# Kernel tuning notes

Measured on AMD Instinct MI355X. Metric: run time of the kernel, lower is better.

## Reference

```python
import jax, jax.numpy as jnp
import numpy as np

H = 768          # hidden_size
NH = 12          # num heads
HD = H // NH     # head dim
NEG = -1e9       # stand-in for -inf masked_fill (numerically safe)


def setup_inputs() -> dict:
    key = jax.random.key(0)
    ks = jax.random.split(key, 8)
    B, T = 4, 2048
    s = 0.02
    return {
        "hidden_states": jax.random.normal(ks[0], (B, T, H), jnp.float32),
        "attention_mask": jnp.zeros((B, 1, 1, T), jnp.float32),
        "Wq": jax.random.normal(ks[1], (H, H), jnp.float32) * s,
        "bq": jnp.zeros((H,), jnp.float32),
        "Wk": jax.random.normal(ks[2], (H, H), jnp.float32) * s,
        "bk": jnp.zeros((H,), jnp.float32),
        "Wv": jax.random.normal(ks[3], (H, H), jnp.float32) * s,
        "bv": jnp.zeros((H,), jnp.float32),
    }


def _split_heads(x):
    b, t, _ = x.shape
    return x.reshape(b, t, NH, HD).transpose(0, 2, 1, 3)  # b h t d


def reference(hidden_states, attention_mask, Wq, bq, Wk, bk, Wv, bv):
    q = _split_heads(hidden_states @ Wq.T + bq)
    k = _split_heads(hidden_states @ Wk.T + bk)
    v = _split_heads(hidden_states @ Wv.T + bv)
    T = q.shape[2]
    scores = jnp.einsum('bhid,bhjd->bhij', q, k) / jnp.sqrt(jnp.float32(HD))
    causal = jnp.tril(jnp.ones((T, T), bool))
    scores = jnp.where(causal, scores, NEG) + attention_mask
    probs = jax.nn.softmax(scores, axis=-1)
    out = jnp.einsum('bhij,bhjd->bhid', probs, v)
    b = out.shape[0]
    return out.transpose(0, 2, 1, 3).reshape(b, T, H)  # b t (h d)
```

## Files before the change

### kernel.cpp

```cpp
#include <hip/hip_runtime.h>
#include <hip/hip_bf16.h>

#define Tsz 2048
#define Hsz 768
#define NHsz 12
#define HDsz 64

typedef unsigned short u16;
typedef unsigned int u32;
typedef __attribute__((ext_vector_type(8))) short bf16x8;
typedef __attribute__((ext_vector_type(4))) float f32x4;
typedef __attribute__((ext_vector_type(4))) u16 u16x4;

__device__ __forceinline__ u16 f2bf(float f) {
    union { __hip_bfloat16 h; u16 u; } c;
    c.h = __float2bfloat16(f);
    return c.u;
}

__device__ __forceinline__ void glds16(const void* src, void* ldsbase) {
    __builtin_amdgcn_global_load_lds(
        (const __attribute__((address_space(1))) u32*)src,
        (__attribute__((address_space(3))) u32*)ldsbase, 16, 0, 0);
}

#define BAR() do { asm volatile("" ::: "memory"); \
                   __builtin_amdgcn_s_barrier();  \
                   asm volatile("" ::: "memory"); } while (0)

#define LDSFRAG(base, row, c) \
    (*(const bf16x8*)((const char*)(base) + (row)*128 + ((((c) << 4)) ^ (((row) & 7) << 4))))

__global__ __launch_bounds__(256) void to_bf16(
    const float* __restrict__ X,
    const float* __restrict__ Wq, const float* __restrict__ Wk,
    const float* __restrict__ Wv,
    u16* __restrict__ xb, u16* __restrict__ wb)
{
    const int bx = blockIdx.x, tid = threadIdx.x;
    const float* src;
    u16* dst;
    size_t off;
    if (bx < 768) {
        src = X; dst = xb;
        off = ((size_t)bx * 256 + tid) * 32;
    } else {
        int r = bx - 768;
        int wsel = r / 72, lr = r % 72;
        src = (wsel == 0) ? Wq : (wsel == 1) ? Wk : Wv;
        dst = wb + (size_t)wsel * (Hsz * Hsz);
        off = ((size_t)lr * 256 + tid) * 32;
    }
    #pragma unroll
    for (int c = 0; c < 4; ++c) {
        float4 a = *(const float4*)(src + off + c * 8);
        float4 b = *(const float4*)(src + off + c * 8 + 4);
        bf16x8 v;
        v[0] = (short)f2bf(a.x); v[1] = (short)f2bf(a.y);
        v[2] = (short)f2bf(a.z); v[3] = (short)f2bf(a.w);
        v[4] = (short)f2bf(b.x); v[5] = (short)f2bf(b.y);
        v[6] = (short)f2bf(b.z); v[7] = (short)f2bf(b.w);
        *(bf16x8*)(dst + off + c * 8) = v;
    }
}

__global__ __launch_bounds__(256) void qkv_gemm(
    const u16* __restrict__ xb, const u16* __restrict__ wb,
    const float* __restrict__ bq, const float* __restrict__ bk,
    const float* __restrict__ bv,
    u16* __restrict__ q_ws, u16* __restrict__ k_ws, u16* __restrict__ vt_ws)
{
    const int tid = threadIdx.x;
    const int w = tid >> 6, l = tid & 63, lg = l >> 4, lh = l & 15;
    const int nb = blockIdx.x;
    const int m0 = blockIdx.y * 128;
    const int z = nb / 6;
    const int n0l = (nb % 6) * 128;
    const u16* Wb = wb + (size_t)z * (Hsz * Hsz);
    const float* bias = (z == 0) ? bq : (z == 1) ? bk : bv;

    __shared__ __align__(16) u16 Xs[2][128 * 64];
    __shared__ __align__(16) u16 Ws[2][128 * 64];

    const int wm = w >> 1, wn = w & 1;

    f32x4 acc[4][4];
    #pragma unroll
    for (int i = 0; i < 4; ++i)
        #pragma unroll
        for (int j = 0; j < 4; ++j)
            acc[i][j] = (f32x4){0.f, 0.f, 0.f, 0.f};

    auto stage = [&](int buf, int k0) {
        #pragma unroll
        for (int p = 0; p < 4; ++p) {
            int id = w * 256 + p * 64 + l;
            int r = id >> 3, c8 = id & 7;
            int cswz = c8 ^ (r & 7);
            glds16(xb + (size_t)(m0 + r) * Hsz + k0 + cswz * 8,
                   &Xs[buf][(w * 256 + p * 64) * 8]);
            glds16(Wb + (size_t)(n0l + r) * Hsz + k0 + cswz * 8,
                   &Ws[buf][(w * 256 + p * 64) * 8]);
        }
    };

    stage(0, 0);
    asm volatile("s_waitcnt vmcnt(0)" ::: "memory");
    BAR();

    #pragma unroll 1
    for (int ks = 0; ks < 12; ++ks) {
        const int cur = ks & 1;
        if (ks < 11) {
            stage(cur ^ 1, (ks + 1) * 64);
            asm volatile("s_waitcnt vmcnt(8)" ::: "memory");
        } else {
            asm volatile("s_waitcnt vmcnt(0)" ::: "memory");
        }
        BAR();

        __builtin_amdgcn_s_setprio(1);
        #pragma unroll
        for (int s = 0; s < 2; ++s) {
            bf16x8 af[4], bfr[4];
            #pragma unroll
            for (int tq = 0; tq < 4; ++tq) {
                af[tq]  = LDSFRAG(Xs[cur], wm * 64 + tq * 16 + lh, 4 * s + lg);
                bfr[tq] = LDSFRAG(Ws[cur], wn * 64 + tq * 16 + lh, 4 * s + lg);
            }
            #pragma unroll
            for (int mt = 0; mt < 4; ++mt)
                #pragma unroll
                for (int nt = 0; nt < 4; ++nt)
                    acc[mt][nt] = __builtin_amdgcn_mfma_f32_16x16x32_bf16(
                        af[mt], bfr[nt], acc[mt][nt], 0, 0, 0);
        }
        __builtin_amdgcn_s_setprio(0);
        BAR();
    }

    #pragma unroll
    for (int nt = 0; nt < 4; ++nt) {
        int nloc = n0l + wn * 64 + nt * 16 + lh;
        float bval = bias[nloc];
        int hh = nloc >> 6, d = nloc & 63;
        #pragma unroll
        for (int mt = 0; mt < 4; ++mt) {
            #pragma unroll
            for (int r = 0; r < 4; ++r) {
                int m = m0 + wm * 64 + mt * 16 + lg * 4 + r;
                int bb = m >> 11, t = m & 2047;
                u16 val = f2bf(acc[mt][nt][r] + bval);
                size_t bh = (size_t)(bb * NHsz + hh);
                if (z == 0)      q_ws[(bh * Tsz + t) * HDsz + d] = val;
                else if (z == 1) k_ws[(bh * Tsz + t) * HDsz + d] = val;
                else             vt_ws[(bh * HDsz + d) * Tsz + t] = val;
            }
        }
    }
}

__global__ __launch_bounds__(256) void attn_mfma(
    const u16* __restrict__ q_ws, const u16* __restrict__ k_ws,
    const u16* __restrict__ vt_ws, const float* __restrict__ am,
    float* __restrict__ out)
{
    const int tid = threadIdx.x;
    const int w = tid >> 6, l = tid & 63, lg = l >> 4, lh = l & 15;
    const int bx = blockIdx.x;
    const int h = blockIdx.y, b = blockIdx.z;
    const int bh = b * NHsz + h;

    const u16* Qb = q_ws + (size_t)bh * Tsz * HDsz;
    const u16* Kb = k_ws + (size_t)bh * Tsz * HDsz;
    const u16* Vb = vt_ws + (size_t)bh * HDsz * Tsz;
    const float* amb = am + (size_t)b * Tsz;

    __shared__ __align__(16) u16 Ks[2][64 * 64];
    __shared__ __align__(16) u16 Vs[2][64 * 64];
    __shared__ __align__(16) u16 Ps[4][16 * 64];
    __shared__ __align__(16) float ambs[Tsz];

    const float LOG2E  = 1.44269504f;
    const float SCALE2 = 0.125f * 1.44269504f;
    const f32x4 zero4 = {0.f, 0.f, 0.f, 0.f};
    u16* myP = &Ps[w][0];
    const int srcbase = l & 0x30;
    const int qo = lg * 4;

    #pragma unroll
    for (int i = 0; i < 2; ++i)
        glds16(amb + (size_t)(i * 256 + tid) * 4, ambs + (i * 256 + w * 64) * 4);
    asm volatile("s_waitcnt vmcnt(0)" ::: "memory");
    __syncthreads();
    #pragma unroll
    for (int i = 0; i < 8; ++i) ambs[tid * 8 + i] *= LOG2E;
    __syncthreads();

    #pragma unroll 1
    for (int ph = 0; ph < 2; ++ph) {
        const int qt = (ph == 0) ? (16 + bx) : (15 - bx);
        const int q0 = qt * 64 + w * 16;
        const int qrow = q0 + lh;

        #pragma unroll
        for (int p = 0; p < 2; ++p) {
            int id = w * 128 + p * 64 + l;
            int r = id >> 3, c8 = id & 7;
            int cswz = c8 ^ (r & 7);
            glds16(Kb + (size_t)r * HDsz + cswz * 8, &Ks[0][(w * 128 + p * 64) * 8]);
            glds16(Vb + (size_t)r * Tsz + cswz * 8, &Vs[0][(w * 128 + p * 64) * 8]);
        }
        bf16x8 qf0 = *(const bf16x8*)(Qb + (size_t)(q0 + lh) * HDsz + lg * 8);
        bf16x8 qf1 = *(const bf16x8*)(Qb + (size_t)(q0 + lh) * HDsz + lg * 8 + 32);
        asm volatile("s_waitcnt vmcnt(0)" ::: "memory");
        BAR();

        f32x4 o[4];
        #pragma unroll
        for (int n = 0; n < 4; ++n) o[n] = zero4;
        float m2 = -1e30f, l2 = 0.f;

        #pragma unroll 1
        for (int kt = 0; kt <= qt; ++kt) {
            const int cur = kt & 1;
            const int kv0 = kt * 64;

            if (kt < qt) {
                const int kv1 = kv0 + 64;
                #pragma unroll
                for (int p = 0; p < 2; ++p) {
                    int id = w * 128 + p * 64 + l;
                    int r = id >> 3, c8 = id & 7;
                    int cswz = c8 ^ (r & 7);
                    glds16(Kb + (size_t)(kv1 + r) * HDsz + cswz * 8,
                           &Ks[cur ^ 1][(w * 128 + p * 64) * 8]);
                    glds16(Vb + (size_t)r * Tsz + kv1 + cswz * 8,
                           &Vs[cur ^ 1][(w * 128 + p * 64) * 8]);
                }
                asm volatile("s_waitcnt vmcnt(4)" ::: "memory");
            } else {
                asm volatile("s_waitcnt vmcnt(0)" ::: "memory");
            }
            BAR();

            const u16* Ksb = &Ks[cur][0];
            const u16* Vsb = &Vs[cur][0];
            const bool diag = (kt == qt);

            f32x4 st[4];
            __builtin_amdgcn_s_setprio(1);
            if (!diag) {
                #pragma unroll
                for (int n = 0; n < 4; ++n) {
                    int row = n * 16 + lh;
                    bf16x8 kf0 = LDSFRAG(Ksb, row, lg);
                    bf16x8 kf1 = LDSFRAG(Ksb, row, 4 + lg);
                    f32x4 c = __builtin_amdgcn_mfma_f32_16x16x32_bf16(kf0, qf0, zero4, 0, 0, 0);
                    st[n] = __builtin_amdgcn_mfma_f32_16x16x32_bf16(kf1, qf1, c, 0, 0, 0);
                }
            } else {
                #pragma unroll
                for (int n = 0; n < 4; ++n) {
                    st[n] = zero4;
                    if (n <= w) {
                        int row = n * 16 + lh;
                        bf16x8 kf0 = LDSFRAG(Ksb, row, lg);
                        bf16x8 kf1 = LDSFRAG(Ksb, row, 4 + lg);
                        f32x4 c = __builtin_amdgcn_mfma_f32_16x16x32_bf16(kf0, qf0, zero4, 0, 0, 0);
                        st[n] = __builtin_amdgcn_mfma_f32_16x16x32_bf16(kf1, qf1, c, 0, 0, 0);
                    }
                }
            }
            __builtin_amdgcn_s_setprio(0);

            float pvv[16];
            float mx = -1e30f;
            if (!diag) {
                #pragma unroll
                for (int n = 0; n < 4; ++n) {
                    f32x4 a4 = *(const f32x4*)(ambs + kv0 + n * 16 + lg * 4);
                    #pragma unroll
                    for (int r = 0; r < 4; ++r) {
                        float sv = fmaf(st[n][r], SCALE2, a4[r]);
                        pvv[n * 4 + r] = sv;
                        mx = fmaxf(mx, sv);
                    }
                }
            } else {
                #pragma unroll
                for (int n = 0; n < 4; ++n) {
                    f32x4 a4 = *(const f32x4*)(ambs + kv0 + n * 16 + lg * 4);
                    #pragma unroll
                    for (int r = 0; r < 4; ++r) {
                        int kvj = kv0 + n * 16 + lg * 4 + r;
                        float sv = (kvj > qrow) ? -1e30f : fmaf(st[n][r], SCALE2, a4[r]);
                        pvv[n * 4 + r] = sv;
                        mx = fmaxf(mx, sv);
                    }
                }
            }
            mx = fmaxf(mx, __shfl_xor(mx, 16));
            mx = fmaxf(mx, __shfl_xor(mx, 32));

            const bool norescale = __all(mx <= m2 + 8.0f);
            float mn = m2;
            if (!norescale) mn = fmaxf(m2, mx);

            float ps = 0.f;
            #pragma unroll
            for (int i = 0; i < 16; ++i) {
                float p = exp2f(pvv[i] - mn);
                pvv[i] = p;
                ps += p;
            }
            ps += __shfl_xor(ps, 16);
            ps += __shfl_xor(ps, 32);

            if (norescale) {
                l2 += ps;
            } else {
                float corr = exp2f(m2 - mn);
                m2 = mn;
                l2 = l2 * corr + ps;
                float co[4];
                #pragma unroll
                for (int r = 0; r < 4; ++r)
                    co[r] = __shfl(corr, srcbase | (qo + r));
                #pragma unroll
                for (int n = 0; n < 4; ++n)
                    #pragma unroll
                    for (int r = 0; r < 4; ++r)
                        o[n][r] *= co[r];
            }

            #pragma unroll
            for (int n = 0; n < 4; ++n) {
                u16x4 v;
                v[0] = f2bf(pvv[n * 4 + 0]); v[1] = f2bf(pvv[n * 4 + 1]);
                v[2] = f2bf(pvv[n * 4 + 2]); v[3] = f2bf(pvv[n * 4 + 3]);
                int chunk = 2 * n + (lg >> 1);
                int byteoff = lh * 128 + ((chunk ^ (lh & 7)) << 4) + ((lg & 1) << 3);
                *(u16x4*)((char*)myP + byteoff) = v;
            }

            const int smaxv = (diag && w < 2) ? 0 : 1;
            __builtin_amdgcn_s_setprio(1);
            #pragma unroll
            for (int s = 0; s < 2; ++s) {
                if (s <= smaxv) {
                    int chunk = (4 * s + lg) ^ (lh & 7);
                    bf16x8 pf = *(const bf16x8*)((const char*)myP + lh * 128 + (chunk << 4));
                    #pragma unroll
                    for (int n = 0; n < 4; ++n) {
                        bf16x8 vf = LDSFRAG(Vsb, n * 16 + lh, 4 * s + lg);
                        o[n] = __builtin_amdgcn_mfma_f32_16x16x32_bf16(pf, vf, o[n], 0, 0, 0);
                    }
                }
            }
            __builtin_amdgcn_s_setprio(0);
            BAR();
        }

        float linv[4];
        #pragma unroll
        for (int r = 0; r < 4; ++r)
            linv[r] = 1.0f / __shfl(l2, srcbase | (qo + r));
        float* ob = out + ((size_t)(b * Tsz + q0 + qo)) * Hsz + h * HDsz + lh;
        #pragma unroll
        for (int r = 0; r < 4; ++r)
            #pragma unroll
            for (int n = 0; n < 4; ++n)
                ob[r * Hsz + n * 16] = o[n][r] * linv[r];
    }
}

extern "C" void kernel_launch(void* const* d_in, const int* in_sizes, int n_in,
                              void* d_out, int out_size, void* d_ws, size_t ws_size,
                              hipStream_t stream) {
    const float* X  = (const float*)d_in[0];
    const float* am = (const float*)d_in[1];
    const float* Wq = (const float*)d_in[2];
    const float* bq = (const float*)d_in[3];
    const float* Wk = (const float*)d_in[4];
    const float* bk = (const float*)d_in[5];
    const float* Wv = (const float*)d_in[6];
    const float* bv = (const float*)d_in[7];
    float* out = (float*)d_out;

    const size_t per = (size_t)8192 * Hsz;
    u16* q_ws  = (u16*)d_ws;
    u16* k_ws  = q_ws + per;
    u16* vt_ws = k_ws + per;

    u16* xb = (u16*)d_out;
    u16* wb = xb + per;

    to_bf16<<<dim3(984), 256, 0, stream>>>(X, Wq, Wk, Wv, xb, wb);

    dim3 g1(18, 64);
    qkv_gemm<<<g1, 256, 0, stream>>>(xb, wb, bq, bk, bv, q_ws, k_ws, vt_ws);

    dim3 g2(16, NHsz, 4);
    attn_mfma<<<g2, 256, 0, stream>>>(q_ws, k_ws, vt_ws, am, out);
}
```

Measured before the change: 150.3 us.

## Redistribute P fragments via cross-lane shuffles and swizzle attention grid mapping

```diff
diff --git a/kernel.cpp b/kernel.cpp
--- a/kernel.cpp
+++ b/kernel.cpp
@@ -167,8 +167,11 @@
 {
     const int tid = threadIdx.x;
     const int w = tid >> 6, l = tid & 63, lg = l >> 4, lh = l & 15;
-    const int bx = blockIdx.x;
-    const int h = blockIdx.y, b = blockIdx.z;
+    const int wg = blockIdx.x;
+    const int swz = (wg & 7) * 96 + (wg >> 3);
+    const int bx = swz & 15;
+    const int grp = swz >> 4;
+    const int h = grp % NHsz, b = grp / NHsz;
     const int bh = b * NHsz + h;
 
     const u16* Qb = q_ws + (size_t)bh * Tsz * HDsz;
@@ -178,15 +181,14 @@
 
     __shared__ __align__(16) u16 Ks[2][64 * 64];
     __shared__ __align__(16) u16 Vs[2][64 * 64];
-    __shared__ __align__(16) u16 Ps[4][16 * 64];
     __shared__ __align__(16) float ambs[Tsz];
 
     const float LOG2E  = 1.44269504f;
     const float SCALE2 = 0.125f * 1.44269504f;
     const f32x4 zero4 = {0.f, 0.f, 0.f, 0.f};
-    u16* myP = &Ps[w][0];
     const int srcbase = l & 0x30;
     const int qo = lg * 4;
+    const int lgb1 = lg >> 1, lgb0 = lg & 1;
 
     #pragma unroll
     for (int i = 0; i < 2; ++i)
@@ -334,31 +336,46 @@
                         o[n][r] *= co[r];
             }
 
+            u32 wAp[4], wBp[4];
             #pragma unroll
             for (int n = 0; n < 4; ++n) {
-                u16x4 v;
-                v[0] = f2bf(pvv[n * 4 + 0]); v[1] = f2bf(pvv[n * 4 + 1]);
-                v[2] = f2bf(pvv[n * 4 + 2]); v[3] = f2bf(pvv[n * 4 + 3]);
-                int chunk = 2 * n + (lg >> 1);
-                int byteoff = lh * 128 + ((chunk ^ (lh & 7)) << 4) + ((lg & 1) << 3);
-                *(u16x4*)((char*)myP + byteoff) = v;
+                wAp[n] = (u32)f2bf(pvv[4 * n + 0]) | ((u32)f2bf(pvv[4 * n + 1]) << 16);
+                wBp[n] = (u32)f2bf(pvv[4 * n + 2]) | ((u32)f2bf(pvv[4 * n + 3]) << 16);
             }
 
             const int smaxv = (diag && w < 2) ? 0 : 1;
-            __builtin_amdgcn_s_setprio(1);
             #pragma unroll
             for (int s = 0; s < 2; ++s) {
                 if (s <= smaxv) {
-                    int chunk = (4 * s + lg) ^ (lh & 7);
-                    bf16x8 pf = *(const bf16x8*)((const char*)myP + lh * 128 + (chunk << 4));
+                    const int n0 = 2 * s, n1 = 2 * s + 1;
+                    u32 sA = lgb1 ? wAp[n0] : wAp[n1];
+                    u32 sB = lgb1 ? wBp[n0] : wBp[n1];
+                    u32 kA = lgb1 ? wAp[n1] : wAp[n0];
+                    u32 kB = lgb1 ? wBp[n1] : wBp[n0];
+                    u32 rA = __shfl_xor(sA, 32);
+                    u32 rB = __shfl_xor(sB, 32);
+                    const bool ownkeep = (lgb1 == lgb0);
+                    u32 s2A = ownkeep ? rA : kA;
+                    u32 s2B = ownkeep ? rB : kB;
+                    u32 fA  = ownkeep ? kA : rA;
+                    u32 fB  = ownkeep ? kB : rB;
+                    u32 r2A = __shfl_xor(s2A, 16);
+                    u32 r2B = __shfl_xor(s2B, 16);
+                    union { u32 u[4]; bf16x8 v; } pk;
+                    pk.u[0] = lgb0 ? r2A : fA;
+                    pk.u[1] = lgb0 ? r2B : fB;
+                    pk.u[2] = lgb0 ? fA : r2A;
+                    pk.u[3] = lgb0 ? fB : r2B;
+                    bf16x8 pf = pk.v;
+                    __builtin_amdgcn_s_setprio(1);
                     #pragma unroll
                     for (int n = 0; n < 4; ++n) {
                         bf16x8 vf = LDSFRAG(Vsb, n * 16 + lh, 4 * s + lg);
                         o[n] = __builtin_amdgcn_mfma_f32_16x16x32_bf16(pf, vf, o[n], 0, 0, 0);
                     }
-                }
-            }
-            __builtin_amdgcn_s_setprio(0);
+                    __builtin_amdgcn_s_setprio(0);
+                }
+            }
             BAR();
         }
 
@@ -401,6 +418,5 @@
     dim3 g1(18, 64);
     qkv_gemm<<<g1, 256, 0, stream>>>(xb, wb, bq, bk, bv, q_ws, k_ws, vt_ws);
 
-    dim3 g2(16, NHsz, 4);
-    attn_mfma<<<g2, 256, 0, stream>>>(q_ws, k_ws, vt_ws, am, out);
-}
+    attn_mfma<<<dim3(768), 256, 0, stream>>>(q_ws, k_ws, vt_ws, am, out);
+}
```

New measurement: 160.2 us. +6.6%, slower.
